# Kernel tuning notes

Hardware: AMD Instinct MI355X
Metric: run time of the kernel (lower is better)

Reference implementation:

```python
import jax, jax.numpy as jnp
import numpy as np

N, E = 100000, 1600000
D_IN, H, C = 128, 4, 32
NEG_SLOPE = 0.2

def setup_inputs() -> dict:
    key = jax.random.key(0)
    ks = jax.random.split(key, 6)
    x = jax.random.normal(ks[0], (N, D_IN), dtype=jnp.float32)
    edge_index = jax.random.randint(ks[1], (2, E), 0, N, dtype=jnp.int64)
    s = 1.0 / np.sqrt(D_IN)
    W_l = jax.random.normal(ks[2], (D_IN, H * C), dtype=jnp.float32) * s
    W_r = jax.random.normal(ks[3], (D_IN, H * C), dtype=jnp.float32) * s
    att = jax.random.normal(ks[4], (H, C), dtype=jnp.float32) * (1.0 / np.sqrt(C))
    bias = jax.random.normal(ks[5], (H * C,), dtype=jnp.float32) * 0.01
    return {"x": x, "edge_index": edge_index, "W_l": W_l, "W_r": W_r, "att": att, "bias": bias}

def reference(x, edge_index, W_l, W_r, att, bias):
    # GATv2: e_ij = att . LeakyReLU(W_l x_j + W_r x_i); softmax over incoming edges of i;
    # out_i = sum_j alpha_ij * (W_l x_j); heads concatenated, then bias.
    src, dst = edge_index[0], edge_index[1]
    n = x.shape[0]
    xl = (x @ W_l).reshape(n, H, C)   # source transform (lin_l)
    xr = (x @ W_r).reshape(n, H, C)   # target transform (lin_r)
    xj = xl[src]                       # [E,H,C] gathered source feats
    xi = xr[dst]                       # [E,H,C] gathered target feats
    e = jax.nn.leaky_relu(xi + xj, NEG_SLOPE)
    score = jnp.einsum('ehc,hc->eh', e, att)          # [E,H]
    # segment softmax over destination nodes
    m = jax.ops.segment_max(score, dst, num_segments=n)  # [N,H]
    ex = jnp.exp(score - m[dst])
    denom = jax.ops.segment_sum(ex, dst, num_segments=n)  # [N,H]
    alpha = ex / (denom[dst] + 1e-16)                      # [E,H]
    out = jax.ops.segment_sum(alpha[..., None] * xj, dst, num_segments=n)  # [N,H,C]
    return out.reshape(n, H * C) + bias
```

## Files before the change

### kernel.cpp

```cpp
#include <hip/hip_runtime.h>
#include <hip/hip_bf16.h>
#include <math.h>

#define N_NODES 100000
#define E_EDGES 1600000
#define D 128
#define NEG_SLOPE 0.2f

#define BSH   8
#define NBKT  391
#define BCAP  4992
#define P1_EPB 8192
#define P1_TPB 512
#define P1_EPT 16

typedef __bf16 bf16x8 __attribute__((ext_vector_type(8)));
typedef float f32x4 __attribute__((ext_vector_type(4)));
typedef float f32x2 __attribute__((ext_vector_type(2)));

__device__ __forceinline__ float bf2f(unsigned short u) {
    union { unsigned int i; float f; } x; x.i = ((unsigned int)u) << 16; return x.f;
}
__device__ __forceinline__ unsigned short f2bf(float f) {
    union { float f; unsigned int i; } x; x.f = f;
    unsigned int r = x.i + 0x7fffu + ((x.i >> 16) & 1u);
    return (unsigned short)(r >> 16);
}
__device__ __forceinline__ void unpack4p(uint2 u, f32x2* lo, f32x2* hi) {
    union { unsigned int i; float f; } a, b, c, d;
    a.i = u.x << 16; b.i = u.x & 0xffff0000u;
    c.i = u.y << 16; d.i = u.y & 0xffff0000u;
    *lo = (f32x2){a.f, b.f}; *hi = (f32x2){c.f, d.f};
}
__device__ __forceinline__ f32x2 pabs(f32x2 v) {
    union { f32x2 f; unsigned int u[2]; } x; x.f = v;
    x.u[0] &= 0x7fffffffu; x.u[1] &= 0x7fffffffu;
    return x.f;
}

__global__ void GATv2Conv_56908316672629_kernel(
    const unsigned int* ei_words, int* flags)
{
    __shared__ int cnt_edge;
    if (threadIdx.x == 0) cnt_edge = 0;
    __syncthreads();
    unsigned int w = ei_words[2 * threadIdx.x + 1];
    if (w != 0u) atomicAdd(&cnt_edge, 1);
    __syncthreads();
    if (threadIdx.x == 0) flags[0] = (cnt_edge == 0) ? 1 : 0;
}

__global__ __launch_bounds__(256) void gemm_f32_kernel(
    const float* __restrict__ X,
    const float* __restrict__ Wl,
    const float* __restrict__ Wr,
    unsigned short* __restrict__ xl, unsigned short* __restrict__ xr)
{
    __shared__ unsigned short Xs[64][136];
    __shared__ unsigned short Wt[128][136];

    const int rowbase = blockIdx.x * 64;
    const int tid = threadIdx.x;

    for (int c = tid; c < 2048; c += 256) {
        int r = c >> 5, k4 = (c & 31) << 2;
        int grow = rowbase + r;
        float4 v = make_float4(0.f, 0.f, 0.f, 0.f);
        if (grow < N_NODES) v = ((const float4*)(X + (size_t)grow * D))[c & 31];
        union { unsigned short us[4]; uint2 u2; } pk;
        pk.us[0] = f2bf(v.x); pk.us[1] = f2bf(v.y);
        pk.us[2] = f2bf(v.z); pk.us[3] = f2bf(v.w);
        *((uint2*)&Xs[r][k4]) = pk.u2;
    }

    const int wave = tid >> 6, lane = tid & 63;
    const int mrow = lane & 15, quad = lane >> 4;

    for (int sel = 0; sel < 2; ++sel) {
        const float* W = sel ? Wr : Wl;
        unsigned short* out = sel ? xr : xl;

        if (sel) __syncthreads();
        for (int c = tid; c < 4096; c += 256) {
            int k = c >> 5, n4 = (c & 31) << 2;
            float4 w = ((const float4*)(W + (size_t)k * D))[c & 31];
            Wt[n4 + 0][k] = f2bf(w.x);
            Wt[n4 + 1][k] = f2bf(w.y);
            Wt[n4 + 2][k] = f2bf(w.z);
            Wt[n4 + 3][k] = f2bf(w.w);
        }
        __syncthreads();

        f32x4 acc[8];
#pragma unroll
        for (int i = 0; i < 8; ++i) acc[i] = (f32x4){0.f, 0.f, 0.f, 0.f};

#pragma unroll
        for (int kk = 0; kk < 4; ++kk) {
            const int k0 = kk * 32 + quad * 8;
            bf16x8 afrag = *(const bf16x8*)&Xs[wave * 16 + mrow][k0];
#pragma unroll
            for (int n0 = 0; n0 < 8; ++n0) {
                bf16x8 bfrag = *(const bf16x8*)&Wt[n0 * 16 + mrow][k0];
                acc[n0] = __builtin_amdgcn_mfma_f32_16x16x32_bf16(afrag, bfrag, acc[n0], 0, 0, 0);
            }
        }

        const int grow0 = rowbase + wave * 16 + quad * 4;
#pragma unroll
        for (int n0 = 0; n0 < 8; ++n0) {
            int col = n0 * 16 + mrow;
#pragma unroll
            for (int r = 0; r < 4; ++r) {
                int grow = grow0 + r;
                if (grow < N_NODES) out[(size_t)grow * D + col] = f2bf(acc[n0][r]);
            }
        }
    }
}

__global__ void zero_kernel(int* p, int n) {
    int i = blockIdx.x * 256 + threadIdx.x;
    if (i < n) p[i] = 0;
}

__device__ __forceinline__ unsigned int edge_word(const unsigned int* ei, int is64,
                                                  long long entry) {
    return is64 ? ei[2 * entry] : ei[entry];
}

__global__ __launch_bounds__(P1_TPB) void bucket_scatter_kernel(
    const unsigned int* __restrict__ ei, const int* __restrict__ flags,
    int* __restrict__ bcur, unsigned int* __restrict__ pairbuf)
{
    __shared__ int h[NBKT];
    __shared__ int gbase[NBKT];

    const int tid = threadIdx.x;
    const int is64 = flags[0];
    const long long e0 = (long long)blockIdx.x * P1_EPB;

    unsigned int sv[P1_EPT], dv[P1_EPT];
#pragma unroll
    for (int j = 0; j < P1_EPT; ++j) {
        long long e = e0 + j * P1_TPB + tid;
        unsigned int s = 0u, d = 0xffffffffu;
        if (e < E_EDGES) {
            s = edge_word(ei, is64, e);
            d = edge_word(ei, is64, (long long)E_EDGES + e);
            if (s >= N_NODES || d >= N_NODES) d = 0xffffffffu;
        }
        sv[j] = s; dv[j] = d;
    }

    for (int i = tid; i < NBKT; i += P1_TPB) h[i] = 0;
    __syncthreads();

#pragma unroll
    for (int j = 0; j < P1_EPT; ++j)
        if (dv[j] != 0xffffffffu) atomicAdd(&h[dv[j] >> BSH], 1);
    __syncthreads();

    for (int i = tid; i < NBKT; i += P1_TPB) {
        int c = h[i];
        gbase[i] = c ? atomicAdd(&bcur[i], c) : 0;
        h[i] = 0;
    }
    __syncthreads();

#pragma unroll
    for (int j = 0; j < P1_EPT; ++j) {
        unsigned int d = dv[j];
        if (d != 0xffffffffu) {
            int b = (int)(d >> BSH);
            int r = gbase[b] + atomicAdd(&h[b], 1);
            if (r < BCAP)
                pairbuf[(size_t)b * BCAP + r] = sv[j] | ((d & 255u) << 24);
        }
    }
}

__global__ __launch_bounds__(256) void bucket_sort_kernel(
    const int* __restrict__ bcur, unsigned int* __restrict__ pairbuf,
    int* __restrict__ rowstart, int* __restrict__ rowend)
{
    __shared__ unsigned int stage[BCAP];
    __shared__ int cnt[256];
    __shared__ int base[256];

    const int b = blockIdx.x;
    const int tid = threadIdx.x;
    int n = bcur[b]; if (n > BCAP) n = BCAP;
    unsigned int* buf = pairbuf + (size_t)b * BCAP;

    for (int i = tid; i < n; i += 256) stage[i] = buf[i];
    cnt[tid] = 0;
    __syncthreads();

    for (int i = tid; i < n; i += 256) atomicAdd(&cnt[stage[i] >> 24], 1);
    __syncthreads();

    int v = cnt[tid];
    base[tid] = v;
    __syncthreads();
    for (int off = 1; off < 256; off <<= 1) {
        int u = (tid >= off) ? base[tid - off] : 0;
        __syncthreads();
        base[tid] += u;
        __syncthreads();
    }
    const int myend = base[tid];
    const int mystart = myend - v;

    const int node = b * 256 + tid;
    if (node < N_NODES) {
        rowstart[node] = b * BCAP + mystart;
        rowend[node]   = b * BCAP + myend;
    }

    cnt[tid] = mystart;
    __syncthreads();

    for (int i = tid; i < n; i += 256) {
        unsigned int p = stage[i];
        int pos = atomicAdd(&cnt[p >> 24], 1);
        buf[pos] = p & 0x00FFFFFFu;
    }
}

__global__ __launch_bounds__(256) void aggregate_kernel(
    const unsigned short* __restrict__ xl, const unsigned short* __restrict__ xr,
    const int* __restrict__ rowstart, const int* __restrict__ rowend,
    const int* __restrict__ ssrc,
    const float* __restrict__ att, const float* __restrict__ bias,
    float* __restrict__ out)
{
    const int t = threadIdx.x & 31;
    const int node = blockIdx.x * 8 + (threadIdx.x >> 5);
    if (node >= N_NODES) return;
    const int f0 = t * 4;

    f32x2 xr0, xr1;
    unpack4p(*(const uint2*)&xr[(size_t)node * D + f0], &xr0, &xr1);
    f32x2 a60 = (f32x2){0.6f * att[f0], 0.6f * att[f0 + 1]};
    f32x2 a61 = (f32x2){0.6f * att[f0 + 2], 0.6f * att[f0 + 3]};
    f32x2 a40 = (f32x2){0.4f * att[f0], 0.4f * att[f0 + 1]};
    f32x2 a41 = (f32x2){0.4f * att[f0 + 2], 0.4f * att[f0 + 3]};

    const uint2* xlp = (const uint2*)xl + (f0 >> 2);

    const int p0 = rowstart[node];
    const int p1 = rowend[node];

    float l = 0.f;
    f32x2 acc0 = (f32x2){0.f, 0.f}, acc1 = (f32x2){0.f, 0.f};

#define ESCORE(u, xa0, xa1, pe)                                   \
    {                                                             \
        unpack4p(u, &xa0, &xa1);                                  \
        f32x2 v0 = xa0 + xr0, v1 = xa1 + xr1;                     \
        f32x2 pp = v0 * a60;                                      \
        pp += pabs(v0) * a40;                                     \
        pp += v1 * a61;                                           \
        pp += pabs(v1) * a41;                                     \
        pe = pp.x + pp.y;                                         \
    }

    int p = p0;
    for (; p + 4 <= p1; p += 4) {
        int s0 = ssrc[p], s1 = ssrc[p + 1], s2 = ssrc[p + 2], s3 = ssrc[p + 3];
        uint2 u0 = xlp[(size_t)s0 * 32];
        uint2 u1 = xlp[(size_t)s1 * 32];
        uint2 u2 = xlp[(size_t)s2 * 32];
        uint2 u3 = xlp[(size_t)s3 * 32];
        f32x2 xa0, xa1, xb0, xb1, xc0, xc1, xd0, xd1;
        float e0, e1, e2, e3;
        ESCORE(u0, xa0, xa1, e0);
        ESCORE(u1, xb0, xb1, e1);
        ESCORE(u2, xc0, xc1, e2);
        ESCORE(u3, xd0, xd1, e3);
#pragma unroll
        for (int off = 1; off < 8; off <<= 1) {
            e0 += __shfl_xor(e0, off);
            e1 += __shfl_xor(e1, off);
            e2 += __shfl_xor(e2, off);
            e3 += __shfl_xor(e3, off);
        }
        float w0 = __expf(e0), w1 = __expf(e1), w2 = __expf(e2), w3 = __expf(e3);
        l += (w0 + w1) + (w2 + w3);
        acc0 += w0 * xa0; acc1 += w0 * xa1;
        acc0 += w1 * xb0; acc1 += w1 * xb1;
        acc0 += w2 * xc0; acc1 += w2 * xc1;
        acc0 += w3 * xd0; acc1 += w3 * xd1;
    }
    for (; p < p1; ++p) {
        int s0 = ssrc[p];
        uint2 u0 = xlp[(size_t)s0 * 32];
        f32x2 xa0, xa1;
        float e0;
        ESCORE(u0, xa0, xa1, e0);
#pragma unroll
        for (int off = 1; off < 8; off <<= 1) e0 += __shfl_xor(e0, off);
        float w0 = __expf(e0);
        l += w0;
        acc0 += w0 * xa0; acc1 += w0 * xa1;
    }
#undef ESCORE

    const float inv = (l > 0.f) ? (1.f / l) : 0.f;
    float4 o;
    o.x = fmaf(acc0.x, inv, bias[f0]);
    o.y = fmaf(acc0.y, inv, bias[f0 + 1]);
    o.z = fmaf(acc1.x, inv, bias[f0 + 2]);
    o.w = fmaf(acc1.y, inv, bias[f0 + 3]);
    *(float4*)&out[(size_t)node * D + f0] = o;
}

extern "C" void kernel_launch(void* const* d_in, const int* in_sizes, int n_in,
                              void* d_out, int out_size, void* d_ws, size_t ws_size,
                              hipStream_t stream)
{
    const float*        X    = (const float*)d_in[0];
    const unsigned int* ei   = (const unsigned int*)d_in[1];
    const float*        Wl   = (const float*)d_in[2];
    const float*        Wr   = (const float*)d_in[3];
    const float*        att  = (const float*)d_in[4];
    const float*        bias = (const float*)d_in[5];

    char* ws = (char*)d_ws;
    size_t off = 0;
    unsigned short* xl = (unsigned short*)(ws + off); off += (size_t)N_NODES * D * 2;
    unsigned short* xr = (unsigned short*)(ws + off); off += (size_t)N_NODES * D * 2;
    unsigned int* pairbuf = (unsigned int*)(ws + off); off += (size_t)NBKT * BCAP * 4;
    int* rowstart = (int*)(ws + off); off += (size_t)N_NODES * 4;
    int* rowend   = (int*)(ws + off); off += (size_t)N_NODES * 4;
    int* bcur     = (int*)(ws + off); off += (size_t)((NBKT + 255) & ~255) * 4;
    int* flags    = (int*)(ws + off); off += 256;

    const int gb = (N_NODES + 63) / 64;
    const int p1b = (E_EDGES + P1_EPB - 1) / P1_EPB;

    GATv2Conv_56908316672629_kernel<<<1, 256, 0, stream>>>(ei, flags);

    gemm_f32_kernel<<<gb, 256, 0, stream>>>(X, Wl, Wr, xl, xr);

    zero_kernel<<<(NBKT + 255) / 256, 256, 0, stream>>>(bcur, NBKT);
    bucket_scatter_kernel<<<p1b, P1_TPB, 0, stream>>>(ei, flags, bcur, pairbuf);
    bucket_sort_kernel<<<NBKT, 256, 0, stream>>>(bcur, pairbuf, rowstart, rowend);

    aggregate_kernel<<<(N_NODES + 7) / 8, 256, 0, stream>>>(
        xl, xr, rowstart, rowend, (const int*)pairbuf, att, bias, (float*)d_out);
}
```

Baseline: 276.2 us.

## Pretranspose weights once, double GEMM tile rows, fuse zeroing, unroll aggregation by eight

The prologue kernel now runs 128 blocks. It zeroes the bucket counters, detects the index width, and converts both weight matrices to transposed bf16 in global memory once. The GEMM no longer rebuilds the transposed weights in LDS per block. It handles 128 rows per block with two accumulator sets that share each B fragment, which is read straight from global/L2. The aggregation loop gains an 8-edge unrolled path for more memory-level parallelism, and att/bias are loaded as float4. Costs are more registers in the GEMM and aggregate kernels, and B fragments now come from global memory instead of LDS.

```diff
diff --git a/kernel.cpp b/kernel.cpp
--- a/kernel.cpp
+++ b/kernel.cpp
@@ -39,30 +39,45 @@
 }
 
 __global__ void GATv2Conv_56908316672629_kernel(
-    const unsigned int* ei_words, int* flags)
+    const unsigned int* ei_words, int* flags,
+    const float* __restrict__ Wl, const float* __restrict__ Wr,
+    unsigned short* __restrict__ wtg, int* __restrict__ bcur)
 {
     __shared__ int cnt_edge;
-    if (threadIdx.x == 0) cnt_edge = 0;
-    __syncthreads();
-    unsigned int w = ei_words[2 * threadIdx.x + 1];
-    if (w != 0u) atomicAdd(&cnt_edge, 1);
-    __syncthreads();
-    if (threadIdx.x == 0) flags[0] = (cnt_edge == 0) ? 1 : 0;
+    const int tid = threadIdx.x;
+    const int bid = blockIdx.x;
+
+    if (bid == 0) {
+        for (int i = tid; i < NBKT; i += 256) bcur[i] = 0;
+    }
+    if (bid == 1) {
+        if (tid == 0) cnt_edge = 0;
+        __syncthreads();
+        unsigned int w = ei_words[2 * tid + 1];
+        if (w != 0u) atomicAdd(&cnt_edge, 1);
+        __syncthreads();
+        if (tid == 0) flags[0] = (cnt_edge == 0) ? 1 : 0;
+    }
+
+    const int gid = bid * 256 + tid;
+    const int sel = gid >> 14;
+    const int rem = gid & 16383;
+    const int k = rem >> 7, n = rem & 127;
+    const float* W = sel ? Wr : Wl;
+    wtg[(size_t)sel * 16384 + n * 128 + k] = f2bf(W[k * 128 + n]);
 }
 
 __global__ __launch_bounds__(256) void gemm_f32_kernel(
     const float* __restrict__ X,
-    const float* __restrict__ Wl,
-    const float* __restrict__ Wr,
+    const unsigned short* __restrict__ wtg,
     unsigned short* __restrict__ xl, unsigned short* __restrict__ xr)
 {
-    __shared__ unsigned short Xs[64][136];
-    __shared__ unsigned short Wt[128][136];
-
-    const int rowbase = blockIdx.x * 64;
+    __shared__ unsigned short Xs[128][136];
+
+    const int rowbase = blockIdx.x * 128;
     const int tid = threadIdx.x;
 
-    for (int c = tid; c < 2048; c += 256) {
+    for (int c = tid; c < 4096; c += 256) {
         int r = c >> 5, k4 = (c & 31) << 2;
         int grow = rowbase + r;
         float4 v = make_float4(0.f, 0.f, 0.f, 0.f);
@@ -72,56 +87,49 @@
         pk.us[2] = f2bf(v.z); pk.us[3] = f2bf(v.w);
         *((uint2*)&Xs[r][k4]) = pk.u2;
     }
+    __syncthreads();
 
     const int wave = tid >> 6, lane = tid & 63;
     const int mrow = lane & 15, quad = lane >> 4;
 
     for (int sel = 0; sel < 2; ++sel) {
-        const float* W = sel ? Wr : Wl;
+        const bf16x8* wt = (const bf16x8*)(wtg + (size_t)sel * 16384);
         unsigned short* out = sel ? xr : xl;
 
-        if (sel) __syncthreads();
-        for (int c = tid; c < 4096; c += 256) {
-            int k = c >> 5, n4 = (c & 31) << 2;
-            float4 w = ((const float4*)(W + (size_t)k * D))[c & 31];
-            Wt[n4 + 0][k] = f2bf(w.x);
-            Wt[n4 + 1][k] = f2bf(w.y);
-            Wt[n4 + 2][k] = f2bf(w.z);
-            Wt[n4 + 3][k] = f2bf(w.w);
-        }
-        __syncthreads();
-
-        f32x4 acc[8];
-#pragma unroll
-        for (int i = 0; i < 8; ++i) acc[i] = (f32x4){0.f, 0.f, 0.f, 0.f};
+        f32x4 accA[8], accB[8];
+#pragma unroll
+        for (int i = 0; i < 8; ++i) {
+            accA[i] = (f32x4){0.f, 0.f, 0.f, 0.f};
+            accB[i] = (f32x4){0.f, 0.f, 0.f, 0.f};
+        }
 
 #pragma unroll
         for (int kk = 0; kk < 4; ++kk) {
             const int k0 = kk * 32 + quad * 8;
-            bf16x8 afrag = *(const bf16x8*)&Xs[wave * 16 + mrow][k0];
+            bf16x8 afA = *(const bf16x8*)&Xs[wave * 16 + mrow][k0];
+            bf16x8 afB = *(const bf16x8*)&Xs[64 + wave * 16 + mrow][k0];
+            const bf16x8* wk = wt + mrow * 16 + kk * 4 + quad;
 #pragma unroll
             for (int n0 = 0; n0 < 8; ++n0) {
-                bf16x8 bfrag = *(const bf16x8*)&Wt[n0 * 16 + mrow][k0];
-                acc[n0] = __builtin_amdgcn_mfma_f32_16x16x32_bf16(afrag, bfrag, acc[n0], 0, 0, 0);
+                bf16x8 bfrag = wk[n0 * 256];
+                accA[n0] = __builtin_amdgcn_mfma_f32_16x16x32_bf16(afA, bfrag, accA[n0], 0, 0, 0);
+                accB[n0] = __builtin_amdgcn_mfma_f32_16x16x32_bf16(afB, bfrag, accB[n0], 0, 0, 0);
             }
         }
 
-        const int grow0 = rowbase + wave * 16 + quad * 4;
+        const int growA = rowbase + wave * 16 + quad * 4;
+        const int growB = growA + 64;
 #pragma unroll
         for (int n0 = 0; n0 < 8; ++n0) {
             int col = n0 * 16 + mrow;
 #pragma unroll
             for (int r = 0; r < 4; ++r) {
-                int grow = grow0 + r;
-                if (grow < N_NODES) out[(size_t)grow * D + col] = f2bf(acc[n0][r]);
+                int ga = growA + r, gb2 = growB + r;
+                if (ga < N_NODES) out[(size_t)ga * D + col] = f2bf(accA[n0][r]);
+                if (gb2 < N_NODES) out[(size_t)gb2 * D + col] = f2bf(accB[n0][r]);
             }
         }
     }
-}
-
-__global__ void zero_kernel(int* p, int n) {
-    int i = blockIdx.x * 256 + threadIdx.x;
-    if (i < n) p[i] = 0;
 }
 
 __device__ __forceinline__ unsigned int edge_word(const unsigned int* ei, int is64,
@@ -242,10 +250,11 @@
 
     f32x2 xr0, xr1;
     unpack4p(*(const uint2*)&xr[(size_t)node * D + f0], &xr0, &xr1);
-    f32x2 a60 = (f32x2){0.6f * att[f0], 0.6f * att[f0 + 1]};
-    f32x2 a61 = (f32x2){0.6f * att[f0 + 2], 0.6f * att[f0 + 3]};
-    f32x2 a40 = (f32x2){0.4f * att[f0], 0.4f * att[f0 + 1]};
-    f32x2 a41 = (f32x2){0.4f * att[f0 + 2], 0.4f * att[f0 + 3]};
+    const float4 av = *(const float4*)&att[f0];
+    f32x2 a60 = (f32x2){0.6f * av.x, 0.6f * av.y};
+    f32x2 a61 = (f32x2){0.6f * av.z, 0.6f * av.w};
+    f32x2 a40 = (f32x2){0.4f * av.x, 0.4f * av.y};
+    f32x2 a41 = (f32x2){0.4f * av.z, 0.4f * av.w};
 
     const uint2* xlp = (const uint2*)xl + (f0 >> 2);
 
@@ -267,6 +276,51 @@
     }
 
     int p = p0;
+    for (; p + 8 <= p1; p += 8) {
+        int s0 = ssrc[p],     s1 = ssrc[p + 1], s2 = ssrc[p + 2], s3 = ssrc[p + 3];
+        int s4 = ssrc[p + 4], s5 = ssrc[p + 5], s6 = ssrc[p + 6], s7 = ssrc[p + 7];
+        uint2 u0 = xlp[(size_t)s0 * 32];
+        uint2 u1 = xlp[(size_t)s1 * 32];
+        uint2 u2 = xlp[(size_t)s2 * 32];
+        uint2 u3 = xlp[(size_t)s3 * 32];
+        uint2 u4 = xlp[(size_t)s4 * 32];
+        uint2 u5 = xlp[(size_t)s5 * 32];
+        uint2 u6 = xlp[(size_t)s6 * 32];
+        uint2 u7 = xlp[(size_t)s7 * 32];
+        f32x2 xa0, xa1, xb0, xb1, xc0, xc1, xd0, xd1;
+        f32x2 xe0, xe1, xf0, xf1, xg0, xg1, xh0, xh1;
+        float e0, e1, e2, e3, e4, e5, e6, e7;
+        ESCORE(u0, xa0, xa1, e0);
+        ESCORE(u1, xb0, xb1, e1);
+        ESCORE(u2, xc0, xc1, e2);
+        ESCORE(u3, xd0, xd1, e3);
+        ESCORE(u4, xe0, xe1, e4);
+        ESCORE(u5, xf0, xf1, e5);
+        ESCORE(u6, xg0, xg1, e6);
+        ESCORE(u7, xh0, xh1, e7);
+#pragma unroll
+        for (int off = 1; off < 8; off <<= 1) {
+            e0 += __shfl_xor(e0, off);
+            e1 += __shfl_xor(e1, off);
+            e2 += __shfl_xor(e2, off);
+            e3 += __shfl_xor(e3, off);
+            e4 += __shfl_xor(e4, off);
+            e5 += __shfl_xor(e5, off);
+            e6 += __shfl_xor(e6, off);
+            e7 += __shfl_xor(e7, off);
+        }
+        float w0 = __expf(e0), w1 = __expf(e1), w2 = __expf(e2), w3 = __expf(e3);
+        float w4 = __expf(e4), w5 = __expf(e5), w6 = __expf(e6), w7 = __expf(e7);
+        l += ((w0 + w1) + (w2 + w3)) + ((w4 + w5) + (w6 + w7));
+        acc0 += w0 * xa0; acc1 += w0 * xa1;
+        acc0 += w1 * xb0; acc1 += w1 * xb1;
+        acc0 += w2 * xc0; acc1 += w2 * xc1;
+        acc0 += w3 * xd0; acc1 += w3 * xd1;
+        acc0 += w4 * xe0; acc1 += w4 * xe1;
+        acc0 += w5 * xf0; acc1 += w5 * xf1;
+        acc0 += w6 * xg0; acc1 += w6 * xg1;
+        acc0 += w7 * xh0; acc1 += w7 * xh1;
+    }
     for (; p + 4 <= p1; p += 4) {
         int s0 = ssrc[p], s1 = ssrc[p + 1], s2 = ssrc[p + 2], s3 = ssrc[p + 3];
         uint2 u0 = xlp[(size_t)s0 * 32];
@@ -308,11 +362,12 @@
 #undef ESCORE
 
     const float inv = (l > 0.f) ? (1.f / l) : 0.f;
+    const float4 bv = *(const float4*)&bias[f0];
     float4 o;
-    o.x = fmaf(acc0.x, inv, bias[f0]);
-    o.y = fmaf(acc0.y, inv, bias[f0 + 1]);
-    o.z = fmaf(acc1.x, inv, bias[f0 + 2]);
-    o.w = fmaf(acc1.y, inv, bias[f0 + 3]);
+    o.x = fmaf(acc0.x, inv, bv.x);
+    o.y = fmaf(acc0.y, inv, bv.y);
+    o.z = fmaf(acc1.x, inv, bv.z);
+    o.w = fmaf(acc1.y, inv, bv.w);
     *(float4*)&out[(size_t)node * D + f0] = o;
 }
 
@@ -336,15 +391,15 @@
     int* rowend   = (int*)(ws + off); off += (size_t)N_NODES * 4;
     int* bcur     = (int*)(ws + off); off += (size_t)((NBKT + 255) & ~255) * 4;
     int* flags    = (int*)(ws + off); off += 256;
-
-    const int gb = (N_NODES + 63) / 64;
+    unsigned short* wtg = (unsigned short*)(ws + off); off += 2 * 128 * 128 * 2;
+
+    const int gb = (N_NODES + 127) / 128;
     const int p1b = (E_EDGES + P1_EPB - 1) / P1_EPB;
 
-    GATv2Conv_56908316672629_kernel<<<1, 256, 0, stream>>>(ei, flags);
-
-    gemm_f32_kernel<<<gb, 256, 0, stream>>>(X, Wl, Wr, xl, xr);
-
-    zero_kernel<<<(NBKT + 255) / 256, 256, 0, stream>>>(bcur, NBKT);
+    GATv2Conv_56908316672629_kernel<<<128, 256, 0, stream>>>(ei, flags, Wl, Wr, wtg, bcur);
+
+    gemm_f32_kernel<<<gb, 256, 0, stream>>>(X, wtg, xl, xr);
+
     bucket_scatter_kernel<<<p1b, P1_TPB, 0, stream>>>(ei, flags, bcur, pairbuf);
     bucket_sort_kernel<<<NBKT, 256, 0, stream>>>(bcur, pairbuf, rowstart, rowend);
 
```

After: 283.5 us. 2.6% more time.
